# Kernel optimization log

Measured on AMD Instinct MI355X. Metric: run time of the kernel, lower is better.

## Reference

```python
import jax, jax.numpy as jnp
import numpy as np

H = 1024; HEADS = 16; DH = 64; W = 256; R = 128; I = 4096
EPS = 1e-5; THETA = 10000.0


def _rms(x, w):
    v = jnp.mean(jnp.square(x.astype(jnp.float32)), axis=-1, keepdims=True)
    return (x * jax.lax.rsqrt(v + EPS)).astype(x.dtype) * w


def _rot_half(x):
    h = x.shape[-1] // 2
    return jnp.concatenate([-x[..., h:], x[..., :h]], axis=-1)


def setup_inputs() -> dict:
    key = jax.random.key(0)
    ks = jax.random.split(key, 6)
    B, S = 2, 4096
    x = jax.random.normal(ks[0], (B, S, H), dtype=jnp.float32)
    position_ids = jnp.tile(jnp.arange(S, dtype=jnp.int32)[None, :], (B, 1))
    sc = 0.02
    return {
        'x': x,
        'position_ids': position_ids,
        'in_norm_w': jnp.ones((H,), jnp.float32),
        'mlp_norm_w': jnp.ones((H,), jnp.float32),
        'qkv_w': jax.random.normal(ks[1], (3 * H, H), jnp.float32) * sc,
        'o_w': jax.random.normal(ks[2], (H, H), jnp.float32) * sc,
        'gate_up_w': jax.random.normal(ks[3], (2 * I, H), jnp.float32) * sc,
        'down_w': jax.random.normal(ks[4], (H, I), jnp.float32) * sc,
        'scorer_w': jax.random.normal(ks[5], (1, H), jnp.float32) * sc,
    }


def reference(x, position_ids, in_norm_w, mlp_norm_w, qkv_w, o_w, gate_up_w, down_w, scorer_w):
    B, S, _ = x.shape
    N = (S - W) // R + 1 if S >= W else 1
    starts = jnp.arange(N) * R                     # [N]
    idx = starts[:, None] + jnp.arange(W)          # [N,W] window gather indices
    w_flat = x[:, idx].reshape(B * N, W, H)        # [BN,W,H]
    p_flat = position_ids[:, idx].reshape(B * N, W)

    # --- windowed causal attention (Phi3-style) ---
    y = _rms(w_flat, in_norm_w)
    qkv = y @ qkv_w.T                              # [BN,W,3H]
    q, k, v = jnp.split(qkv, 3, axis=-1)
    def heads(t):
        return t.reshape(B * N, W, HEADS, DH).transpose(0, 2, 1, 3)  # [BN,h,W,d]
    q, k, v = heads(q), heads(k), heads(v)
    inv_freq = 1.0 / (THETA ** (jnp.arange(0, DH, 2, dtype=jnp.float32) / DH))
    freqs = p_flat.astype(jnp.float32)[..., None] * inv_freq        # [BN,W,d/2]
    emb = jnp.concatenate([freqs, freqs], axis=-1)                  # [BN,W,d]
    cos = jnp.cos(emb)[:, None]; sin = jnp.sin(emb)[:, None]        # [BN,1,W,d]
    q = q * cos + _rot_half(q) * sin
    k = k * cos + _rot_half(k) * sin
    scores = jnp.einsum('bhqd,bhkd->bhqk', q, k) / jnp.sqrt(jnp.float32(DH))
    causal = jnp.tril(jnp.ones((W, W), bool))
    scores = jnp.where(causal, scores, jnp.finfo(scores.dtype).min)
    attn = jax.nn.softmax(scores, axis=-1)
    o = jnp.einsum('bhqk,bhkd->bhqd', attn, v)
    o = o.transpose(0, 2, 1, 3).reshape(B * N, W, H) @ o_w.T
    y = w_flat + o

    # --- MLP (SwiGLU, gate first then up, per Phi3MLP) ---
    y2 = _rms(y, mlp_norm_w)
    gu = y2 @ gate_up_w.T
    g, u = jnp.split(gu, 2, axis=-1)
    y2 = (u * jax.nn.silu(g)) @ down_w.T
    y = y + y2
    y_win = y.reshape(B, N, W, H)

    # --- attn-pool summary per window ---
    score = jnp.einsum('bnwh,h->bnw', y_win, scorer_w[0])
    alpha = jax.nn.softmax(score, axis=-1)
    z_blocks = jnp.einsum('bnw,bnwh->bnh', alpha, y_win)

    # --- triangular overlap-add stitch ---
    up = jnp.linspace(0.0, 1.0, W // 2 + 1)
    blend = jnp.concatenate([up[:-1], up[::-1]])[:W]                # [W]
    y_acc = jnp.zeros((B, S, H), x.dtype).at[:, idx].add(y_win * blend[None, None, :, None])
    w_acc = jnp.zeros((B, S), x.dtype).at[:, idx].add(jnp.broadcast_to(blend, (N, W)))
    y_local = y_acc / (w_acc[..., None] + 1e-8)

    block_pos = jnp.broadcast_to(starts + (W - 1), (B, N))
    return y_local, z_blocks, block_pos
```

## Files before the change

kernel.cpp:

```cpp
#include <hip/hip_runtime.h>
#include <hip/hip_fp16.h>
#include <math.h>

#define HDIM 1024
#define WWIN 256
#define RSTRIDE 128
#define NWIN 31
#define SEQ 4096
#define MROWS 15872
#define IDIM 4096
#define BN_TOT 62

#define GLOBAL_AS __attribute__((address_space(1)))
#define LDS_AS    __attribute__((address_space(3)))

typedef _Float16 f16x8 __attribute__((ext_vector_type(8)));
typedef float f32x4 __attribute__((ext_vector_type(4)));

__global__ __launch_bounds__(256) void conv_h(const float* __restrict__ s,
        __half* __restrict__ d, int n)
{
    int i = (blockIdx.x * 256 + threadIdx.x) * 8;
    if (i >= n) return;
    float4 a = *(const float4*)(s + i);
    float4 b = *(const float4*)(s + i + 4);
    uint4 o; __half* h = (__half*)&o;
    h[0]=__float2half(a.x); h[1]=__float2half(a.y); h[2]=__float2half(a.z); h[3]=__float2half(a.w);
    h[4]=__float2half(b.x); h[5]=__float2half(b.y); h[6]=__float2half(b.z); h[7]=__float2half(b.w);
    *(uint4*)(d + i) = o;
}

__global__ __launch_bounds__(256) void rope_table(const int* __restrict__ pos,
        float* __restrict__ tab)
{
    int idx = blockIdx.x * 256 + threadIdx.x;
    int bs = idx >> 5, j = idx & 31;
    float pf = (float)pos[bs];
    float invf = powf(10000.0f, -(float)j * (1.0f/32.0f));
    float sn, cs;
    sincosf(pf * invf, &sn, &cs);
    tab[(size_t)bs*64 + j] = cs;
    tab[(size_t)bs*64 + 32 + j] = sn;
}

template<bool GATHER>
__global__ __launch_bounds__(256) void rms_kernel(const float* __restrict__ src,
        const float* __restrict__ wnorm, __half* __restrict__ dst, int bn0)
{
    int lrow = blockIdx.x;
    const float* in;
    if (GATHER) {
        int grow = bn0 * WWIN + lrow;
        int bn = grow >> 8, wo = grow & 255;
        int b = bn / NWIN, n = bn % NWIN;
        in = src + ((size_t)b*SEQ + n*RSTRIDE + wo) * HDIM;
    } else {
        in = src + (size_t)lrow * HDIM;
    }
    int t = threadIdx.x;
    float4 v = *(const float4*)(in + t*4);
    float ss = v.x*v.x + v.y*v.y + v.z*v.z + v.w*v.w;
    #pragma unroll
    for (int off = 32; off > 0; off >>= 1) ss += __shfl_xor(ss, off);
    __shared__ float wsum[4];
    int wv = t >> 6;
    if ((t & 63) == 0) wsum[wv] = ss;
    __syncthreads();
    float tot = wsum[0] + wsum[1] + wsum[2] + wsum[3];
    float rs = 1.0f / sqrtf(tot * (1.0f/1024.0f) + 1e-5f);
    float4 wv4 = *(const float4*)(wnorm + t*4);
    uint2 pack; __half* hp = (__half*)&pack;
    hp[0] = __float2half(v.x*rs*wv4.x);
    hp[1] = __float2half(v.y*rs*wv4.y);
    hp[2] = __float2half(v.z*rs*wv4.z);
    hp[3] = __float2half(v.w*rs*wv4.w);
    *(uint2*)(dst + (size_t)lrow*HDIM + t*4) = pack;
}

template<int MODE>
__global__ __launch_bounds__(256) void gemm_h(const __half* __restrict__ A,
        const __half* __restrict__ Bw, void* __restrict__ Cv,
        const float* __restrict__ X, int M, int N, int K, int bn0)
{
    __shared__ __half As[128*32];
    __shared__ __half Bs[128*32];
    int t = threadIdx.x;
    int lane = t & 63, wv = t >> 6;
    int wr = wv >> 1, wc = wv & 1;
    int m0 = blockIdx.y * 128, n0 = blockIdx.x * 128;
    int fr = lane & 15, fq = lane >> 4;

    int srow0 = wv * 32;
    int lr = lane >> 2;
    int lcs = lane & 3;
    f32x4 acc[4][4] = {};

    for (int k0 = 0; k0 < K; k0 += 32) {
        #pragma unroll
        for (int j = 0; j < 2; ++j) {
            int r = srow0 + j*16 + lr;
            int ks = (lcs ^ ((r >> 1) & 3)) << 3;
            __builtin_amdgcn_global_load_lds(
                (const GLOBAL_AS void*)(A + (size_t)(m0 + r) * K + k0 + ks),
                (LDS_AS void*)(As + (srow0 + j*16) * 32), 16, 0, 0);
            __builtin_amdgcn_global_load_lds(
                (const GLOBAL_AS void*)(Bw + (size_t)(n0 + r) * K + k0 + ks),
                (LDS_AS void*)(Bs + (srow0 + j*16) * 32), 16, 0, 0);
        }
        __syncthreads();
        f16x8 af[4], bf[4];
        #pragma unroll
        for (int i = 0; i < 4; ++i) {
            int row = wr*64 + i*16 + fr;
            af[i] = *(const f16x8*)(As + row*32 + ((fq ^ ((row >> 1) & 3)) << 3));
        }
        #pragma unroll
        for (int j2 = 0; j2 < 4; ++j2) {
            int row = wc*64 + j2*16 + fr;
            bf[j2] = *(const f16x8*)(Bs + row*32 + ((fq ^ ((row >> 1) & 3)) << 3));
        }
        #pragma unroll
        for (int i = 0; i < 4; ++i)
            #pragma unroll
            for (int j2 = 0; j2 < 4; ++j2)
                acc[i][j2] = __builtin_amdgcn_mfma_f32_16x16x32_f16(af[i], bf[j2], acc[i][j2], 0, 0, 0);
        __syncthreads();
    }

    int rq = (lane >> 4) * 4;
    int cl = lane & 15;
    #pragma unroll
    for (int i = 0; i < 4; ++i) {
        #pragma unroll
        for (int q = 0; q < 4; ++q) {
            int m = m0 + wr*64 + i*16 + rq + q;
            const float* xr = nullptr;
            if (MODE == 2) {
                int grow = bn0 * WWIN + m;
                int bn = grow >> 8, wo = grow & 255;
                int bb = bn / NWIN, nn = bn % NWIN;
                xr = X + ((size_t)bb*SEQ + nn*RSTRIDE + wo) * HDIM;
            }
            #pragma unroll
            for (int j = 0; j < 4; ++j) {
                int col = n0 + wc*64 + j*16 + cl;
                float v = acc[i][j][q];
                if (MODE == 0) {
                    ((float*)Cv)[(size_t)m*N + col] = v;
                } else if (MODE == 1) {
                    ((__half*)Cv)[(size_t)m*N + col] = __float2half(v);
                } else if (MODE == 2) {
                    ((float*)Cv)[(size_t)m*N + col] = v + xr[col];
                } else {
                    float* cp = (float*)Cv + (size_t)m*N + col;
                    *cp = *cp + v;
                }
            }
        }
    }
}

__global__ __launch_bounds__(256) void silu_mul(const __half* __restrict__ gu,
        __half* __restrict__ hid)
{
    int m = blockIdx.x, t = threadIdx.x;
    const __half* gp = gu + (size_t)m*8192 + t*16;
    const __half* up = gp + 4096;
    __half* hp = hid + (size_t)m*4096 + t*16;
    #pragma unroll
    for (int s = 0; s < 2; ++s) {
        uint4 gv = *(const uint4*)(gp + s*8);
        uint4 uv = *(const uint4*)(up + s*8);
        const __half* g8 = (const __half*)&gv;
        const __half* u8 = (const __half*)&uv;
        uint4 ov; __half* o8 = (__half*)&ov;
        #pragma unroll
        for (int e = 0; e < 8; ++e) {
            float g = __half2float(g8[e]);
            float u = __half2float(u8[e]);
            o8[e] = __float2half(u * g / (1.0f + expf(-g)));
        }
        *(uint4*)(hp + s*8) = ov;
    }
}

__global__ __launch_bounds__(256) void attn_mfma(const __half* __restrict__ qkv,
        const float* __restrict__ ropet, __half* __restrict__ out, int bn0)
{
    __shared__ __half K_s[256][72];
    __shared__ __half Vt_s[64][264];
    __shared__ __half P_s[4][64][72];

    int bid = blockIdx.x;
    int h = bid & 15, lbn = bid >> 4;
    int gbn = bn0 + lbn;
    int b = gbn / NWIN, n = gbn % NWIN;
    int t = threadIdx.x, wv = t >> 6, lane = t & 63;
    int fr = lane & 15, fq = lane >> 4;

    const __half* base = qkv + (size_t)(lbn * WWIN) * 3072 + h * 64;
    const float* tb = ropet + ((size_t)b * SEQ + n * RSTRIDE) * 64;

    {
        int r = t;
        const __half* kp = base + (size_t)r * 3072 + 1024;
        const float* tr = tb + (size_t)r * 64;
        #pragma unroll
        for (int d0 = 0; d0 < 32; d0 += 4) {
            float4 c4 = *(const float4*)(tr + d0);
            float4 s4 = *(const float4*)(tr + 32 + d0);
            uint2 lo2 = *(const uint2*)(kp + d0);
            uint2 hi2 = *(const uint2*)(kp + 32 + d0);
            const __half* lo = (const __half*)&lo2;
            const __half* hi = (const __half*)&hi2;
            const float* cc = (const float*)&c4;
            const float* sn = (const float*)&s4;
            uint2 olo, ohi; __half* plo = (__half*)&olo; __half* phi = (__half*)&ohi;
            #pragma unroll
            for (int e = 0; e < 4; ++e) {
                float lv = __half2float(lo[e]), hv = __half2float(hi[e]);
                plo[e] = __float2half(lv*cc[e] - hv*sn[e]);
                phi[e] = __float2half(hv*cc[e] + lv*sn[e]);
            }
            *(uint2*)&K_s[r][d0] = olo;
            *(uint2*)&K_s[r][32 + d0] = ohi;
        }
        const __half* vp = base + (size_t)r * 3072 + 2048;
        #pragma unroll
        for (int d0 = 0; d0 < 64; d0 += 8) {
            uint4 v8 = *(const uint4*)(vp + d0);
            const __half* ve = (const __half*)&v8;
            #pragma unroll
            for (int e = 0; e < 8; ++e) Vt_s[d0 + e][r] = ve[e];
        }
    }
    {
        int r = wv * 64 + lane;
        const __half* qp = base + (size_t)r * 3072;
        const float* tr = tb + (size_t)r * 64;
        #pragma unroll
        for (int d0 = 0; d0 < 32; d0 += 4) {
            float4 c4 = *(const float4*)(tr + d0);
            float4 s4 = *(const float4*)(tr + 32 + d0);
            uint2 lo2 = *(const uint2*)(qp + d0);
            uint2 hi2 = *(const uint2*)(qp + 32 + d0);
            const __half* lo = (const __half*)&lo2;
            const __half* hi = (const __half*)&hi2;
            const float* cc = (const float*)&c4;
            const float* sn = (const float*)&s4;
            uint2 olo, ohi; __half* plo = (__half*)&olo; __half* phi = (__half*)&ohi;
            #pragma unroll
            for (int e = 0; e < 4; ++e) {
                float lv = __half2float(lo[e]), hv = __half2float(hi[e]);
                plo[e] = __float2half(lv*cc[e] - hv*sn[e]);
                phi[e] = __float2half(hv*cc[e] + lv*sn[e]);
            }
            *(uint2*)&P_s[wv][lane][d0] = olo;
            *(uint2*)&P_s[wv][lane][32 + d0] = ohi;
        }
    }
    __syncthreads();

    f16x8 qf[4][2];
    #pragma unroll
    for (int i = 0; i < 4; ++i)
        #pragma unroll
        for (int kk = 0; kk < 2; ++kk)
            qf[i][kk] = *(const f16x8*)&P_s[wv][i*16 + fr][kk*32 + fq*8];
    __builtin_amdgcn_sched_barrier(0);

    f32x4 Oacc[4][4] = {};
    float mrow[4][4], lrow[4][4];
    #pragma unroll
    for (int i = 0; i < 4; ++i)
        #pragma unroll
        for (int q = 0; q < 4; ++q) { mrow[i][q] = -3.0e38f; lrow[i][q] = 0.f; }

    for (int kb = 0; kb <= wv; ++kb) {
        f16x8 kf[4][2];
        #pragma unroll
        for (int j = 0; j < 4; ++j)
            #pragma unroll
            for (int kk = 0; kk < 2; ++kk)
                kf[j][kk] = *(const f16x8*)&K_s[kb*64 + j*16 + fr][kk*32 + fq*8];
        f32x4 sacc[4][4] = {};
        #pragma unroll
        for (int i = 0; i < 4; ++i)
            #pragma unroll
            for (int j = 0; j < 4; ++j) {
                sacc[i][j] = __builtin_amdgcn_mfma_f32_16x16x32_f16(qf[i][0], kf[j][0], sacc[i][j], 0, 0, 0);
                sacc[i][j] = __builtin_amdgcn_mfma_f32_16x16x32_f16(qf[i][1], kf[j][1], sacc[i][j], 0, 0, 0);
            }
        bool diag = (kb == wv);
        #pragma unroll
        for (int i = 0; i < 4; ++i)
            #pragma unroll
            for (int j = 0; j < 4; ++j)
                #pragma unroll
                for (int q = 0; q < 4; ++q) {
                    float v = sacc[i][j][q] * 0.125f;
                    if (diag && (j*16 + fr) > (i*16 + fq*4 + q)) v = -3.0e38f;
                    sacc[i][j][q] = v;
                }
        #pragma unroll
        for (int i = 0; i < 4; ++i) {
            #pragma unroll
            for (int q = 0; q < 4; ++q) {
                float bm = fmaxf(fmaxf(sacc[i][0][q], sacc[i][1][q]),
                                 fmaxf(sacc[i][2][q], sacc[i][3][q]));
                #pragma unroll
                for (int off = 1; off < 16; off <<= 1) bm = fmaxf(bm, __shfl_xor(bm, off));
                float mn = fmaxf(mrow[i][q], bm);
                float alpha = __expf(mrow[i][q] - mn);
                mrow[i][q] = mn;
                float rs = 0.f;
                #pragma unroll
                for (int j = 0; j < 4; ++j) {
                    float p = __expf(sacc[i][j][q] - mn);
                    sacc[i][j][q] = p;
                    rs += p;
                }
                #pragma unroll
                for (int off = 1; off < 16; off <<= 1) rs += __shfl_xor(rs, off);
                lrow[i][q] = lrow[i][q] * alpha + rs;
                #pragma unroll
                for (int j = 0; j < 4; ++j) Oacc[i][j][q] *= alpha;
            }
        }
        #pragma unroll
        for (int i = 0; i < 4; ++i)
            #pragma unroll
            for (int j = 0; j < 4; ++j)
                #pragma unroll
                for (int q = 0; q < 4; ++q)
                    P_s[wv][i*16 + fq*4 + q][j*16 + fr] = __float2half(sacc[i][j][q]);
        __builtin_amdgcn_sched_barrier(0);
        f16x8 pa[4][2], vb[4][2];
        #pragma unroll
        for (int i = 0; i < 4; ++i)
            #pragma unroll
            for (int kk = 0; kk < 2; ++kk)
                pa[i][kk] = *(const f16x8*)&P_s[wv][i*16 + fr][kk*32 + fq*8];
        #pragma unroll
        for (int j = 0; j < 4; ++j)
            #pragma unroll
            for (int kk = 0; kk < 2; ++kk)
                vb[j][kk] = *(const f16x8*)&Vt_s[j*16 + fr][kb*64 + kk*32 + fq*8];
        #pragma unroll
        for (int i = 0; i < 4; ++i)
            #pragma unroll
            for (int j = 0; j < 4; ++j) {
                Oacc[i][j] = __builtin_amdgcn_mfma_f32_16x16x32_f16(pa[i][0], vb[j][0], Oacc[i][j], 0, 0, 0);
                Oacc[i][j] = __builtin_amdgcn_mfma_f32_16x16x32_f16(pa[i][1], vb[j][1], Oacc[i][j], 0, 0, 0);
            }
        __builtin_amdgcn_sched_barrier(0);
    }

    #pragma unroll
    for (int i = 0; i < 4; ++i)
        #pragma unroll
        for (int q = 0; q < 4; ++q) {
            float inv = 1.0f / lrow[i][q];
            #pragma unroll
            for (int j = 0; j < 4; ++j)
                P_s[wv][i*16 + fq*4 + q][j*16 + fr] = __float2half(Oacc[i][j][q] * inv);
        }
    __builtin_amdgcn_sched_barrier(0);
    {
        int rl = lane >> 3, c0 = (lane & 7) * 8;
        #pragma unroll
        for (int it = 0; it < 8; ++it) {
            int row = it*8 + rl;
            uint4 v = *(const uint4*)&P_s[wv][row][c0];
            *(uint4*)&out[((size_t)(lbn*WWIN + wv*64 + row)) * HDIM + h*64 + c0] = v;
        }
    }
}

__global__ __launch_bounds__(256) void scorer_kernel(const float* __restrict__ y,
        const float* __restrict__ sw, float* __restrict__ zout, float* __restrict__ pout)
{
    int bn = blockIdx.x;
    int t = threadIdx.x, wv = t >> 6, lane = t & 63;
    __shared__ float sc[256];
    __shared__ float red[8];
    const float* yb = y + (size_t)bn * WWIN * HDIM;

    for (int w = wv*64; w < wv*64 + 64; ++w) {
        const float* row = yb + (size_t)w * HDIM;
        float s = 0.f;
        #pragma unroll
        for (int c = 0; c < 4; ++c) {
            int o = lane*4 + c*256;
            float4 v = *(const float4*)(row + o);
            float4 q = *(const float4*)(sw + o);
            s += v.x*q.x + v.y*q.y + v.z*q.z + v.w*q.w;
        }
        #pragma unroll
        for (int off = 32; off > 0; off >>= 1) s += __shfl_xor(s, off);
        if (lane == 0) sc[w] = s;
    }
    __syncthreads();
    float v = sc[t];
    float m = v;
    #pragma unroll
    for (int off = 32; off > 0; off >>= 1) m = fmaxf(m, __shfl_xor(m, off));
    if (lane == 0) red[wv] = m;
    __syncthreads();
    m = fmaxf(fmaxf(red[0], red[1]), fmaxf(red[2], red[3]));
    float e = expf(v - m);
    float s = e;
    #pragma unroll
    for (int off = 32; off > 0; off >>= 1) s += __shfl_xor(s, off);
    if (lane == 0) red[4 + wv] = s;
    __syncthreads();
    float tot = red[4] + red[5] + red[6] + red[7];
    float alpha = e / tot;
    sc[t] = alpha;
    __syncthreads();
    float4 acc = make_float4(0.f, 0.f, 0.f, 0.f);
    for (int w = 0; w < 256; ++w) {
        float a = sc[w];
        float4 v4 = *(const float4*)(yb + (size_t)w*HDIM + t*4);
        acc.x += a*v4.x; acc.y += a*v4.y; acc.z += a*v4.z; acc.w += a*v4.w;
    }
    *(float4*)(zout + (size_t)bn*HDIM + t*4) = acc;
    if (t == 0) pout[bn] = (float)((bn % NWIN)*RSTRIDE + (WWIN - 1));
}

__global__ __launch_bounds__(256) void stitch_kernel(const float* __restrict__ y,
        float* __restrict__ out)
{
    int gid = blockIdx.x;
    int b = gid >> 12, s = gid & 4095;
    int t = threadIdx.x;
    int nmin = (s < 256) ? 0 : ((s - 128) >> 7);
    int nmax = s >> 7; if (nmax > NWIN - 1) nmax = NWIN - 1;
    float4 acc = make_float4(0.f, 0.f, 0.f, 0.f);
    float wsum = 0.f;
    for (int n = nmin; n <= nmax; ++n) {
        int w = s - n * RSTRIDE;
        float wt = ((w < 128) ? (float)w : (float)(256 - w)) * 0.0078125f;
        const float* row = y + ((size_t)(b*NWIN + n)*WWIN + w)*HDIM + t*4;
        float4 v = *(const float4*)row;
        acc.x += wt*v.x; acc.y += wt*v.y; acc.z += wt*v.z; acc.w += wt*v.w;
        wsum += wt;
    }
    float inv = 1.0f / (wsum + 1e-8f);
    *(float4*)(out + ((size_t)b*SEQ + s)*HDIM + t*4) =
        make_float4(acc.x*inv, acc.y*inv, acc.z*inv, acc.w*inv);
}

extern "C" void kernel_launch(void* const* d_in, const int* in_sizes, int n_in,
                              void* d_out, int out_size, void* d_ws, size_t ws_size,
                              hipStream_t stream)
{
    const float* x    = (const float*)d_in[0];
    const int*   pos  = (const int*)d_in[1];
    const float* inw  = (const float*)d_in[2];
    const float* mlpw = (const float*)d_in[3];
    const float* qkvw = (const float*)d_in[4];
    const float* ow   = (const float*)d_in[5];
    const float* guw  = (const float*)d_in[6];
    const float* dww  = (const float*)d_in[7];
    const float* scw  = (const float*)d_in[8];
    float* out = (float*)d_out;

    const size_t FIXED = (size_t)MROWS*HDIM*4
        + ((size_t)3072*1024 + 1024*1024 + 8192*1024 + 1024*4096)*2
        + (size_t)2*SEQ*64*4;
    const int cands[10] = {31, 24, 20, 16, 14, 12, 10, 8, 4, 2};
    int chbn = 1;
    for (int i = 0; i < 10; ++i) {
        size_t need = FIXED + (size_t)cands[i]*256*26624;
        if (need <= ws_size) { chbn = cands[i]; break; }
    }

    char* p = (char*)d_ws;
    float*  y1     = (float*)p;   p += (size_t)MROWS*HDIM*4;
    __half* qkvw_h = (__half*)p;  p += (size_t)3072*1024*2;
    __half* ow_h   = (__half*)p;  p += (size_t)1024*1024*2;
    __half* guw_h  = (__half*)p;  p += (size_t)8192*1024*2;
    __half* dww_h  = (__half*)p;  p += (size_t)1024*4096*2;
    float*  ropet  = (float*)p;   p += (size_t)2*SEQ*64*4;
    size_t mcMax = (size_t)chbn * 256;
    __half* reg1   = (__half*)p;  p += mcMax*1024*2;
    char*   reg2   = p;           p += mcMax*16384;
    __half* hidden = (__half*)p;

    conv_h<<<3072*1024/2048, 256, 0, stream>>>(qkvw, qkvw_h, 3072*1024);
    conv_h<<<1024*1024/2048, 256, 0, stream>>>(ow,   ow_h,   1024*1024);
    conv_h<<<8192*1024/2048, 256, 0, stream>>>(guw,  guw_h,  8192*1024);
    conv_h<<<1024*4096/2048, 256, 0, stream>>>(dww,  dww_h,  1024*4096);
    rope_table<<<2*SEQ*32/256, 256, 0, stream>>>(pos, ropet);

    for (int c0 = 0; c0 < BN_TOT; c0 += chbn) {
        int nb = (BN_TOT - c0 < chbn) ? (BN_TOT - c0) : chbn;
        int mc = nb * WWIN;
        float*  y1c   = y1 + (size_t)c0 * WWIN * HDIM;
        __half* ynorm = reg1, *attnb = reg1, *y2n = reg1;
        __half* qkvb  = (__half*)reg2;
        __half* gu    = (__half*)reg2;

        rms_kernel<true><<<mc, 256, 0, stream>>>(x, inw, ynorm, c0);
        gemm_h<1><<<dim3(24, mc/128), 256, 0, stream>>>(ynorm, qkvw_h, qkvb, nullptr, mc, 3072, 1024, 0);
        attn_mfma<<<nb*16, 256, 0, stream>>>(qkvb, ropet, attnb, c0);
        gemm_h<2><<<dim3(8, mc/128), 256, 0, stream>>>(attnb, ow_h, y1c, x, mc, 1024, 1024, c0);
        rms_kernel<false><<<mc, 256, 0, stream>>>(y1c, mlpw, y2n, 0);
        gemm_h<1><<<dim3(64, mc/128), 256, 0, stream>>>(y2n, guw_h, gu, nullptr, mc, 8192, 1024, 0);
        silu_mul<<<mc, 256, 0, stream>>>(gu, hidden);
        gemm_h<3><<<dim3(8, mc/128), 256, 0, stream>>>(hidden, dww_h, y1c, nullptr, mc, 1024, 4096, 0);
    }
    scorer_kernel<<<BN_TOT, 256, 0, stream>>>(y1, scw, out + 8388608, out + 8452096);
    stitch_kernel<<<2*SEQ, 256, 0, stream>>>(y1, out);
}
```

Before: 1.373 ms.

## Fuse SwiGLU activation into gate/up GEMM epilogue with interleaved weight tiles

Replaces the separate gate_up GEMM plus silu_mul kernel with one GEMM. Each block computes 64 gate columns and the matching 64 up columns by loading interleaved rows of the weight matrix. The gate half writes silu(g) to LDS and the up half multiplies it in and stores the fp16 hidden activation directly. This removes the round trip of the full 8192-wide gate/up intermediate through global memory, shrinking the workspace so larger chunks fit, at the cost of a reduced effective N-tile per block and an extra LDS exchange.

```diff
diff --git a/kernel.cpp b/kernel.cpp
--- a/kernel.cpp
+++ b/kernel.cpp
@@ -145,9 +145,7 @@
             for (int j = 0; j < 4; ++j) {
                 int col = n0 + wc*64 + j*16 + cl;
                 float v = acc[i][j][q];
-                if (MODE == 0) {
-                    ((float*)Cv)[(size_t)m*N + col] = v;
-                } else if (MODE == 1) {
+                if (MODE == 1) {
                     ((__half*)Cv)[(size_t)m*N + col] = __float2half(v);
                 } else if (MODE == 2) {
                     ((float*)Cv)[(size_t)m*N + col] = v + xr[col];
@@ -160,27 +158,85 @@
     }
 }
 
-__global__ __launch_bounds__(256) void silu_mul(const __half* __restrict__ gu,
-        __half* __restrict__ hid)
-{
-    int m = blockIdx.x, t = threadIdx.x;
-    const __half* gp = gu + (size_t)m*8192 + t*16;
-    const __half* up = gp + 4096;
-    __half* hp = hid + (size_t)m*4096 + t*16;
-    #pragma unroll
-    for (int s = 0; s < 2; ++s) {
-        uint4 gv = *(const uint4*)(gp + s*8);
-        uint4 uv = *(const uint4*)(up + s*8);
-        const __half* g8 = (const __half*)&gv;
-        const __half* u8 = (const __half*)&uv;
-        uint4 ov; __half* o8 = (__half*)&ov;
-        #pragma unroll
-        for (int e = 0; e < 8; ++e) {
-            float g = __half2float(g8[e]);
-            float u = __half2float(u8[e]);
-            o8[e] = __float2half(u * g / (1.0f + expf(-g)));
-        }
-        *(uint4*)(hp + s*8) = ov;
+__global__ __launch_bounds__(256) void gemm_gu(const __half* __restrict__ A,
+        const __half* __restrict__ Bw, __half* __restrict__ Hid, int M, int K)
+{
+    __shared__ float exbuf[128*66];
+    __half* As = (__half*)exbuf;
+    __half* Bs = (__half*)exbuf + 128*32;
+    int t = threadIdx.x;
+    int lane = t & 63, wv = t >> 6;
+    int wr = wv >> 1, wc = wv & 1;
+    int m0 = blockIdx.y * 128, n0 = blockIdx.x * 64;
+    int fr = lane & 15, fq = lane >> 4;
+
+    int srow0 = wv * 32;
+    int lr = lane >> 2;
+    int lcs = lane & 3;
+    f32x4 acc[4][4] = {};
+
+    for (int k0 = 0; k0 < K; k0 += 32) {
+        #pragma unroll
+        for (int j = 0; j < 2; ++j) {
+            int r = srow0 + j*16 + lr;
+            int ks = (lcs ^ ((r >> 1) & 3)) << 3;
+            int gr = (r & 64) ? (IDIM + n0 + (r & 63)) : (n0 + r);
+            __builtin_amdgcn_global_load_lds(
+                (const GLOBAL_AS void*)(A + (size_t)(m0 + r) * K + k0 + ks),
+                (LDS_AS void*)(As + (srow0 + j*16) * 32), 16, 0, 0);
+            __builtin_amdgcn_global_load_lds(
+                (const GLOBAL_AS void*)(Bw + (size_t)gr * K + k0 + ks),
+                (LDS_AS void*)(Bs + (srow0 + j*16) * 32), 16, 0, 0);
+        }
+        __syncthreads();
+        f16x8 af[4], bf[4];
+        #pragma unroll
+        for (int i = 0; i < 4; ++i) {
+            int row = wr*64 + i*16 + fr;
+            af[i] = *(const f16x8*)(As + row*32 + ((fq ^ ((row >> 1) & 3)) << 3));
+        }
+        #pragma unroll
+        for (int j2 = 0; j2 < 4; ++j2) {
+            int row = wc*64 + j2*16 + fr;
+            bf[j2] = *(const f16x8*)(Bs + row*32 + ((fq ^ ((row >> 1) & 3)) << 3));
+        }
+        #pragma unroll
+        for (int i = 0; i < 4; ++i)
+            #pragma unroll
+            for (int j2 = 0; j2 < 4; ++j2)
+                acc[i][j2] = __builtin_amdgcn_mfma_f32_16x16x32_f16(af[i], bf[j2], acc[i][j2], 0, 0, 0);
+        __syncthreads();
+    }
+
+    int rq = (lane >> 4) * 4;
+    int cl = lane & 15;
+    if (wc == 0) {
+        #pragma unroll
+        for (int i = 0; i < 4; ++i)
+            #pragma unroll
+            for (int q = 0; q < 4; ++q) {
+                int row = wr*64 + i*16 + rq + q;
+                #pragma unroll
+                for (int j = 0; j < 4; ++j) {
+                    float g = acc[i][j][q];
+                    exbuf[row*66 + j*16 + cl] = g / (1.0f + expf(-g));
+                }
+            }
+    }
+    __syncthreads();
+    if (wc == 1) {
+        #pragma unroll
+        for (int i = 0; i < 4; ++i)
+            #pragma unroll
+            for (int q = 0; q < 4; ++q) {
+                int row = wr*64 + i*16 + rq + q;
+                int m = m0 + row;
+                #pragma unroll
+                for (int j = 0; j < 4; ++j) {
+                    float sg = exbuf[row*66 + j*16 + cl];
+                    Hid[(size_t)m*IDIM + n0 + j*16 + cl] = __float2half(acc[i][j][q] * sg);
+                }
+            }
     }
 }
 
@@ -472,7 +528,7 @@
     const int cands[10] = {31, 24, 20, 16, 14, 12, 10, 8, 4, 2};
     int chbn = 1;
     for (int i = 0; i < 10; ++i) {
-        size_t need = FIXED + (size_t)cands[i]*256*26624;
+        size_t need = FIXED + (size_t)cands[i]*256*16384;
         if (need <= ws_size) { chbn = cands[i]; break; }
     }
 
@@ -485,7 +541,7 @@
     float*  ropet  = (float*)p;   p += (size_t)2*SEQ*64*4;
     size_t mcMax = (size_t)chbn * 256;
     __half* reg1   = (__half*)p;  p += mcMax*1024*2;
-    char*   reg2   = p;           p += mcMax*16384;
+    __half* qkvb   = (__half*)p;  p += mcMax*3072*2;
     __half* hidden = (__half*)p;
 
     conv_h<<<3072*1024/2048, 256, 0, stream>>>(qkvw, qkvw_h, 3072*1024);
@@ -499,16 +555,13 @@
         int mc = nb * WWIN;
         float*  y1c   = y1 + (size_t)c0 * WWIN * HDIM;
         __half* ynorm = reg1, *attnb = reg1, *y2n = reg1;
-        __half* qkvb  = (__half*)reg2;
-        __half* gu    = (__half*)reg2;
 
         rms_kernel<true><<<mc, 256, 0, stream>>>(x, inw, ynorm, c0);
         gemm_h<1><<<dim3(24, mc/128), 256, 0, stream>>>(ynorm, qkvw_h, qkvb, nullptr, mc, 3072, 1024, 0);
         attn_mfma<<<nb*16, 256, 0, stream>>>(qkvb, ropet, attnb, c0);
         gemm_h<2><<<dim3(8, mc/128), 256, 0, stream>>>(attnb, ow_h, y1c, x, mc, 1024, 1024, c0);
         rms_kernel<false><<<mc, 256, 0, stream>>>(y1c, mlpw, y2n, 0);
-        gemm_h<1><<<dim3(64, mc/128), 256, 0, stream>>>(y2n, guw_h, gu, nullptr, mc, 8192, 1024, 0);
-        silu_mul<<<mc, 256, 0, stream>>>(gu, hidden);
+        gemm_gu<<<dim3(64, mc/128), 256, 0, stream>>>(y2n, guw_h, hidden, mc, 1024);
         gemm_h<3><<<dim3(8, mc/128), 256, 0, stream>>>(hidden, dww_h, y1c, nullptr, mc, 1024, 4096, 0);
     }
     scorer_kernel<<<BN_TOT, 256, 0, stream>>>(y1, scw, out + 8388608, out + 8452096);
```

Result: faster. 1.179 ms (-14.1%).
